# Performance work log

Hardware: AMD Instinct MI355X
Metric: run time of the kernel (lower is better)

The kernel has to match this reference:

```python
import jax, jax.numpy as jnp
import numpy as np

H, F = 4, 32          # num_of_heads, num_out_features
HF = H * F            # 128
F_IN = 128
EDGE_DIM = 64
HIDDEN = 256
B = 64
MLE = 1500
N = B * MLE           # 96000
E = 600000
LN_EPS = 1e-5


def setup_inputs() -> dict:
    key = jax.random.key(0)
    ks = jax.random.split(key, 20)

    def glorot(k, shape):
        fan_in, fan_out = shape[-2], shape[-1]
        lim = np.sqrt(6.0 / (fan_in + fan_out))
        return jax.random.uniform(k, shape, jnp.float32, -lim, lim)

    inp = {
        "in_nodes_features": jax.random.normal(ks[0], (N, F_IN), jnp.float32),
        "edge_index": jax.random.randint(ks[1], (2, E), 0, N),
        "edges": jax.random.normal(ks[2], (E, EDGE_DIM), jnp.float32),
        "instructions": jax.random.normal(ks[3], (B, HIDDEN), jnp.float32),
        "batch_ids": jax.random.randint(ks[4], (E,), 0, B),
        "max_local_entity": MLE,
        # parameters (stored as [in, out]; torch Linear is x @ W.T)
        "W_proj": glorot(ks[5], (F_IN, HF)),
        "W_edge": glorot(ks[6], (EDGE_DIM, HF)),
        "W_src_ins": glorot(ks[7], (HIDDEN, HF)),
        "b_src_ins": jnp.zeros((HF,), jnp.float32),
        "W_trg_ins": glorot(ks[8], (HIDDEN, HF)),
        "b_trg_ins": jnp.zeros((HF,), jnp.float32),
        "W_edge_ins": glorot(ks[9], (HIDDEN, HF)),
        "b_edge_ins": jnp.zeros((HF,), jnp.float32),
        "a_src": glorot(ks[10], (1, H, F)),
        "a_trg": glorot(ks[11], (1, H, F)),
        "a_edge": glorot(ks[12], (1, H, F)),
        "bias": jnp.zeros((HF,), jnp.float32),
        "W_skip": glorot(ks[13], (F_IN, HF)),
        "ln_gamma": jnp.ones((2 * HF,), jnp.float32),
        "ln_beta": jnp.zeros((2 * HF,), jnp.float32),
    }
    return inp


def _segment_softmax(scores, seg_idx, num_nodes):
    # scores: [E, H]; softmax over edges sharing the same seg_idx node
    s = scores - jax.lax.stop_gradient(scores.max())  # global-max shift, as in original
    e = jnp.exp(s)
    denom = jax.ops.segment_sum(e, seg_idx, num_segments=num_nodes)  # [N, H]
    return (e / (denom[seg_idx] + 1e-16))[..., None]  # [E, H, 1]


def _branch(proj, lift_idx, agg_idx, scores_per_edge, x, W_skip, bias, num_nodes):
    att = _segment_softmax(scores_per_edge, agg_idx, num_nodes)          # [E,H,1]
    weighted = proj[lift_idx] * att                                      # [E,H,F]
    out = jax.ops.segment_sum(weighted, agg_idx, num_segments=num_nodes) # [N,H,F]
    out = out + (x @ W_skip).reshape(num_nodes, H, F)                    # skip (F != F_in path)
    out = out.reshape(num_nodes, HF) + bias                              # concat heads + bias
    return out


def reference(in_nodes_features, edge_index, edges, instructions, batch_ids,
              max_local_entity, W_proj, W_edge, W_src_ins, b_src_ins,
              W_trg_ins, b_trg_ins, W_edge_ins, b_edge_ins,
              a_src, a_trg, a_edge, bias, W_skip, ln_gamma, ln_beta):
    x = in_nodes_features                      # dropout disabled (eval / p=0)
    num_nodes = x.shape[0]
    b = instructions.shape[0]
    src_idx, trg_idx = edge_index[0], edge_index[1]

    proj = (x @ W_proj).reshape(num_nodes, H, F)           # [N,H,F]
    eproj = (edges @ W_edge).reshape(-1, H, F)             # [E,H,F]

    def bridge(Wi, bi):  # instruction -> per-node [N,H,F]
        br = instructions @ Wi + bi                        # [B,HF]
        br = jnp.broadcast_to(br[:, None, :], (b, max_local_entity, HF))
        return br.reshape(num_nodes, H, F)

    src_br = bridge(W_src_ins, b_src_ins)
    trg_br = bridge(W_trg_ins, b_trg_ins)
    edge_br = (instructions @ W_edge_ins + b_edge_ins)[batch_ids].reshape(-1, H, F)

    scores_source = (proj * a_src * src_br).sum(-1)        # [N,H]
    scores_target = (proj * a_trg * trg_br).sum(-1)        # [N,H]
    scores_edge = (eproj * a_edge * edge_br).sum(-1)       # [E,H]

    scores_per_edge = jax.nn.leaky_relu(
        scores_source[src_idx] + scores_target[trg_idx] + scores_edge,
        negative_slope=0.2)                                # [E,H]

    # direction == 'all': aggregate src->trg and trg->src
    trg_feats = _branch(proj, src_idx, trg_idx, scores_per_edge, x, W_skip, bias, num_nodes)
    src_feats = _branch(proj, trg_idx, src_idx, scores_per_edge, x, W_skip, bias, num_nodes)

    out = jnp.concatenate([src_feats, trg_feats], axis=1)  # [N, 2*HF]
    mu = out.mean(-1, keepdims=True)
    var = ((out - mu) ** 2).mean(-1, keepdims=True)
    return (out - mu) * jax.lax.rsqrt(var + LN_EPS) * ln_gamma + ln_beta
```

## Files before the change

kernel.cpp:

```cpp
#include <hip/hip_runtime.h>
#include <stdint.h>

typedef unsigned short ushortT;
typedef __attribute__((ext_vector_type(8))) short short8;
typedef __attribute__((ext_vector_type(4))) float float4_;

#define HH 4
#define FF 32
#define HFD 128
#define F_IN 128
#define EDGE_DIM 64
#define HIDDEN 256
#define BB 64
#define MLE 1500
#define NN 96000
#define EEc 600000
#define CAP 32

__device__ __forceinline__ float bf_lo(uint32_t u){ return __uint_as_float(u << 16); }
__device__ __forceinline__ float bf_hi(uint32_t u){ return __uint_as_float(u & 0xffff0000u); }
__device__ __forceinline__ uint32_t f2bf(float f){
    uint32_t u = __float_as_uint(f);
    return (u + 0x7fffu + ((u >> 16) & 1u)) >> 16;
}
__device__ __forceinline__ short8 cvt8(const float* p){
    float4_ x0 = *(const float4_*)p;
    float4_ x1 = *(const float4_*)(p + 4);
    short8 r;
    r[0]=(short)f2bf(x0[0]); r[1]=(short)f2bf(x0[1]); r[2]=(short)f2bf(x0[2]); r[3]=(short)f2bf(x0[3]);
    r[4]=(short)f2bf(x1[0]); r[5]=(short)f2bf(x1[1]); r[6]=(short)f2bf(x1[2]); r[7]=(short)f2bf(x1[3]);
    return r;
}

__global__ void k_bridge(const float* ins, const float* Wsrc, const float* bsrc,
                         const float* Wtrg, const float* btrg,
                         const float* Wedg, const float* bedg,
                         const float* a_src, const float* a_trg, const float* a_edge,
                         const float* W_edge,
                         float* csrc, float* ctrg, float* Mout)
{
    __shared__ float ins_s[HIDDEN];
    __shared__ float ce_s[HFD];
    int b = blockIdx.x, t = threadIdx.x;
    const float* ip = ins + b * HIDDEN;
    ins_s[t]       = ip[t];
    ins_s[t + 128] = ip[t + 128];
    __syncthreads();
    float as = 0.f, at = 0.f, ae = 0.f;
    #pragma unroll 8
    for (int k = 0; k < HIDDEN; k++){
        float iv = ins_s[k];
        as += iv * Wsrc[k*HFD + t];
        at += iv * Wtrg[k*HFD + t];
        ae += iv * Wedg[k*HFD + t];
    }
    csrc[b*HFD + t] = (as + bsrc[t]) * a_src[t];
    ctrg[b*HFD + t] = (at + btrg[t]) * a_trg[t];
    ce_s[t] = (ae + bedg[t]) * a_edge[t];
    __syncthreads();
    #pragma unroll
    for (int rep = 0; rep < 2; rep++){
        int idx = t + rep * 128;
        int d = idx >> 2, h = idx & 3;
        float acc = 0.f;
        #pragma unroll
        for (int f = 0; f < FF; f++)
            acc += W_edge[d*HFD + h*FF + f] * ce_s[h*FF + f];
        Mout[b*256 + h*64 + d] = acc;
    }
}

__global__ void k_transpose(const float* Wp, const float* Wsk, ushortT* WcatT)
{
    int idx = blockIdx.x * 256 + threadIdx.x;
    int c = idx >> 7;
    int d = idx & 127;
    float v = (c < 128) ? Wp[d*128 + c] : Wsk[d*128 + (c - 128)];
    WcatT[c*128 + d] = (ushortT)f2bf(v);
}

__global__ __launch_bounds__(256) void k_gemm(const float* x, const ushortT* WcatT,
                                              const float* csrc, const float* ctrg,
                                              ushortT* proj, ushortT* skip,
                                              float* s_src, float* s_trg)
{
    int t = threadIdx.x;
    int w = t >> 6, lane = t & 63;
    int q = lane >> 4, n16 = lane & 15;
    size_t node = (size_t)blockIdx.x * 64 + w * 16 + n16;

    float4_ acc[16];
    #pragma unroll
    for (int j = 0; j < 16; j++) acc[j] = (float4_){0.f, 0.f, 0.f, 0.f};

    #pragma unroll
    for (int kk = 0; kk < 4; kk++){
        short8 bfrag = cvt8(x + node * 128 + kk*32 + q*8);
        #pragma unroll
        for (int j = 0; j < 16; j++){
            short8 afrag = *(const short8*)(WcatT + (size_t)(j*16 + n16) * 128 + kk*32 + q*8);
            acc[j] = __builtin_amdgcn_mfma_f32_16x16x32_bf16(afrag, bfrag, acc[j], 0, 0, 0);
        }
    }

    #pragma unroll
    for (int j = 0; j < 16; j++){
        uint32_t p0 = f2bf(acc[j][0]) | (f2bf(acc[j][1]) << 16);
        uint32_t p1 = f2bf(acc[j][2]) | (f2bf(acc[j][3]) << 16);
        ushortT* base = (j < 8) ? (proj + node*128 + j*16 + q*4)
                                : (skip + node*128 + (j-8)*16 + q*4);
        uint2 pv; pv.x = p0; pv.y = p1;
        *(uint2*)base = pv;
    }

    int b = (int)(node / MLE);
    const float* cs = csrc + b * HFD;
    const float* ct = ctrg + b * HFD;
    float ps[4] = {0,0,0,0}, pt[4] = {0,0,0,0};
    #pragma unroll
    for (int j = 0; j < 8; j++){
        int h = j >> 1;
        #pragma unroll
        for (int r = 0; r < 4; r++){
            int c = j*16 + q*4 + r;
            ps[h] += acc[j][r] * cs[c];
            pt[h] += acc[j][r] * ct[c];
        }
    }
    #pragma unroll
    for (int m = 16; m < 64; m <<= 1){
        #pragma unroll
        for (int hh = 0; hh < 4; hh++){
            ps[hh] += __shfl_xor(ps[hh], m, 64);
            pt[hh] += __shfl_xor(pt[hh], m, 64);
        }
    }
    float vs = (q == 0) ? ps[0] : (q == 1) ? ps[1] : (q == 2) ? ps[2] : ps[3];
    float vt = (q == 0) ? pt[0] : (q == 1) ? pt[1] : (q == 2) ? pt[2] : pt[3];
    s_src[node*4 + q] = vs;
    s_trg[node*4 + q] = vt;
}

__global__ __launch_bounds__(256) void k_score(const int* eidx, const int* bids,
    const float* edges, const float* M, const float* s_src, const float* s_trg,
    uint4* recs)
{
    int t = threadIdx.x;
    int wave = t >> 6, l = t & 63;
    int g = l >> 4, s = l & 15;
    int eb = (blockIdx.x * 4 + wave) * 16;

    int i_sel = s >> 2;
    int h_sel = s & 3;
    int e   = eb + i_sel*4 + g;
    int src = eidx[e];
    int trg = eidx[EEc + e];
    float ssv = s_src[(size_t)src*4 + h_sel];
    float stv = s_trg[(size_t)trg*4 + h_sel];

    float4_ ev[4];
    int bidv[4];
    #pragma unroll
    for (int i = 0; i < 4; i++){
        int r = i*4 + g;
        ev[i]   = *(const float4_*)(edges + (size_t)(eb + r) * 64 + s*4);
        bidv[i] = bids[eb + r];
    }

    float p00=0.f,p01=0.f,p02=0.f,p03=0.f;
    float p10=0.f,p11=0.f,p12=0.f,p13=0.f;
    float p20=0.f,p21=0.f,p22=0.f,p23=0.f;
    float p30=0.f,p31=0.f,p32=0.f,p33=0.f;
    #pragma unroll
    for (int i = 0; i < 4; i++){
        const float* Mb = M + (size_t)bidv[i] * 256;
        float4_ m0 = *(const float4_*)(Mb +   0 + s*4);
        float4_ m1 = *(const float4_*)(Mb +  64 + s*4);
        float4_ m2 = *(const float4_*)(Mb + 128 + s*4);
        float4_ m3 = *(const float4_*)(Mb + 192 + s*4);
        float4_ e4 = ev[i];
        float d0 = e4[0]*m0[0] + e4[1]*m0[1] + e4[2]*m0[2] + e4[3]*m0[3];
        float d1 = e4[0]*m1[0] + e4[1]*m1[1] + e4[2]*m1[2] + e4[3]*m1[3];
        float d2 = e4[0]*m2[0] + e4[1]*m2[1] + e4[2]*m2[2] + e4[3]*m2[3];
        float d3 = e4[0]*m3[0] + e4[1]*m3[1] + e4[2]*m3[2] + e4[3]*m3[3];
        if (i == 0){ p00=d0; p01=d1; p02=d2; p03=d3; }
        if (i == 1){ p10=d0; p11=d1; p12=d2; p13=d3; }
        if (i == 2){ p20=d0; p21=d1; p22=d2; p23=d3; }
        if (i == 3){ p30=d0; p31=d1; p32=d2; p33=d3; }
    }

    #pragma unroll
    for (int mm = 1; mm < 16; mm <<= 1){
        p00 += __shfl_xor(p00, mm, 64); p01 += __shfl_xor(p01, mm, 64);
        p02 += __shfl_xor(p02, mm, 64); p03 += __shfl_xor(p03, mm, 64);
        p10 += __shfl_xor(p10, mm, 64); p11 += __shfl_xor(p11, mm, 64);
        p12 += __shfl_xor(p12, mm, 64); p13 += __shfl_xor(p13, mm, 64);
        p20 += __shfl_xor(p20, mm, 64); p21 += __shfl_xor(p21, mm, 64);
        p22 += __shfl_xor(p22, mm, 64); p23 += __shfl_xor(p23, mm, 64);
        p30 += __shfl_xor(p30, mm, 64); p31 += __shfl_xor(p31, mm, 64);
        p32 += __shfl_xor(p32, mm, 64); p33 += __shfl_xor(p33, mm, 64);
    }

    float q0 = h_sel==0 ? p00 : h_sel==1 ? p01 : h_sel==2 ? p02 : p03;
    float q1 = h_sel==0 ? p10 : h_sel==1 ? p11 : h_sel==2 ? p12 : p13;
    float q2 = h_sel==0 ? p20 : h_sel==1 ? p21 : h_sel==2 ? p22 : p23;
    float q3 = h_sel==0 ? p30 : h_sel==1 ? p31 : h_sel==2 ? p32 : p33;
    float se = i_sel==0 ? q0 : i_sel==1 ? q1 : i_sel==2 ? q2 : q3;

    float sc = ssv + stv + se;
    sc = sc > 0.f ? sc : 0.2f * sc;
    float exv = __expf(sc);

    uint32_t my   = f2bf(exv) << ((h_sel & 1) * 16);
    uint32_t pair = my | __shfl_xor(my, 1, 64);
    uint32_t both = __shfl_xor(pair, 2, 64);

    if (h_sel == 0){
        uint4 rec;
        rec.x = (uint32_t)src; rec.y = (uint32_t)trg;
        rec.z = pair; rec.w = both;
        recs[e] = rec;
    }
}

__global__ __launch_bounds__(256) void k_build(const int* eidx,
    int* cnt_src, int* cnt_trg, uint32_t* adj_src, uint32_t* adj_trg)
{
    int e = blockIdx.x * 256 + threadIdx.x;
    if (e >= EEc) return;
    int src = eidx[e];
    int trg = eidx[EEc + e];
    int sl = atomicAdd(&cnt_src[src], 1);
    if (sl < CAP) adj_src[(size_t)src*CAP + sl] = (uint32_t)e;
    int sl2 = atomicAdd(&cnt_trg[trg], 1);
    if (sl2 < CAP) adj_trg[(size_t)trg*CAP + sl2] = (uint32_t)e;
}

__global__ __launch_bounds__(256) void k_agg(const ushortT* proj, const ushortT* skip,
    const float* bias,
    const int* cnt_src, const int* cnt_trg,
    const uint32_t* adj_src, const uint32_t* adj_trg, const uint4* recs,
    const float* gamma, const float* beta, float* out)
{
    __shared__ int   sh_nbr[2][4][CAP];
    __shared__ float sh_ev [2][4][CAP*4];

    int wave = threadIdx.x >> 6, lane = threadIdx.x & 63;
    int n = blockIdx.x * 4 + wave;
    int h = lane >> 4;

    int cnt0 = cnt_src[n]; if (cnt0 > CAP) cnt0 = CAP;
    int cnt1 = cnt_trg[n]; if (cnt1 > CAP) cnt1 = CAP;

    uint32_t e0 = 0, e1 = 0;
    if (lane < cnt0) e0 = adj_src[(size_t)n * CAP + lane];
    if (lane < cnt1) e1 = adj_trg[(size_t)n * CAP + lane];
    if (lane < cnt0){
        uint4 rec = recs[e0];
        sh_nbr[0][wave][lane] = (int)rec.y;
        float4_ evv = { bf_lo(rec.z), bf_hi(rec.z), bf_lo(rec.w), bf_hi(rec.w) };
        *(float4_*)&sh_ev[0][wave][lane*4] = evv;
    }
    if (lane < cnt1){
        uint4 rec = recs[e1];
        sh_nbr[1][wave][lane] = (int)rec.x;
        float4_ evv = { bf_lo(rec.z), bf_hi(rec.z), bf_lo(rec.w), bf_hi(rec.w) };
        *(float4_*)&sh_ev[1][wave][lane*4] = evv;
    }

    uint32_t sv = ((const uint32_t*)(skip + (size_t)n * 128))[lane];
    float b0 = bias[2*lane], b1 = bias[2*lane + 1];

    __syncthreads();

    float sk0 = bf_lo(sv) + b0;
    float sk1 = bf_hi(sv) + b1;

    float a0 = 0.f, a1 = 0.f, ad = 0.f;
    #pragma unroll 4
    for (int i = 0; i < cnt0; i++){
        int nbr  = sh_nbr[0][wave][i];
        float evw = sh_ev[0][wave][i*4 + h];
        uint32_t pv = ((const uint32_t*)(proj + (size_t)nbr * 128))[lane];
        a0 += evw * bf_lo(pv);
        a1 += evw * bf_hi(pv);
        ad += evw;
    }
    float inv = 1.f / (ad + 1e-16f);
    float f0 = a0 * inv + sk0;
    float f1 = a1 * inv + sk1;

    a0 = 0.f; a1 = 0.f; ad = 0.f;
    #pragma unroll 4
    for (int i = 0; i < cnt1; i++){
        int nbr  = sh_nbr[1][wave][i];
        float evw = sh_ev[1][wave][i*4 + h];
        uint32_t pv = ((const uint32_t*)(proj + (size_t)nbr * 128))[lane];
        a0 += evw * bf_lo(pv);
        a1 += evw * bf_hi(pv);
        ad += evw;
    }
    inv = 1.f / (ad + 1e-16f);
    float f2 = a0 * inv + sk0;
    float f3 = a1 * inv + sk1;

    float sum = f0 + f1 + f2 + f3;
    float sq  = f0*f0 + f1*f1 + f2*f2 + f3*f3;
    #pragma unroll
    for (int m = 1; m < 64; m <<= 1){
        sum += __shfl_xor(sum, m, 64);
        sq  += __shfl_xor(sq,  m, 64);
    }
    float mu  = sum * (1.f/256.f);
    float var = sq * (1.f/256.f) - mu*mu;
    var = var < 0.f ? 0.f : var;
    float rr = rsqrtf(var + 1e-5f);

    float o0 = (f0 - mu) * rr * gamma[2*lane]           + beta[2*lane];
    float o1 = (f1 - mu) * rr * gamma[2*lane + 1]       + beta[2*lane + 1];
    float o2 = (f2 - mu) * rr * gamma[128 + 2*lane]     + beta[128 + 2*lane];
    float o3 = (f3 - mu) * rr * gamma[128 + 2*lane + 1] + beta[128 + 2*lane + 1];

    float* orow = out + (size_t)n * 256;
    *(float2*)(orow + 2*lane)       = make_float2(o0, o1);
    *(float2*)(orow + 128 + 2*lane) = make_float2(o2, o3);
}

extern "C" void kernel_launch(void* const* d_in, const int* in_sizes, int n_in,
                              void* d_out, int out_size, void* d_ws, size_t ws_size,
                              hipStream_t stream)
{
    const float* x      = (const float*)d_in[0];
    const int*   eidx   = (const int*)d_in[1];
    const float* edges  = (const float*)d_in[2];
    const float* ins    = (const float*)d_in[3];
    const int*   bids   = (const int*)d_in[4];
    const float* Wproj  = (const float*)d_in[6];
    const float* Wedge  = (const float*)d_in[7];
    const float* Wsrc   = (const float*)d_in[8];
    const float* bsrc   = (const float*)d_in[9];
    const float* Wtrg   = (const float*)d_in[10];
    const float* btrg   = (const float*)d_in[11];
    const float* Wedgi  = (const float*)d_in[12];
    const float* bedgi  = (const float*)d_in[13];
    const float* a_src  = (const float*)d_in[14];
    const float* a_trg  = (const float*)d_in[15];
    const float* a_edge = (const float*)d_in[16];
    const float* bias   = (const float*)d_in[17];
    const float* Wskip  = (const float*)d_in[18];
    const float* gamma  = (const float*)d_in[19];
    const float* beta   = (const float*)d_in[20];

    char* ws = (char*)d_ws;
    size_t off = 0;
    ushortT* proj  = (ushortT*)(ws + off); off += (size_t)NN * 128 * 2;
    ushortT* skip  = (ushortT*)(ws + off); off += (size_t)NN * 128 * 2;
    ushortT* WcatT = (ushortT*)(ws + off); off += 256 * 128 * 2;
    float*   csrc  = (float*)(ws + off);   off += BB * HFD * 4;
    float*   ctrg  = (float*)(ws + off);   off += BB * HFD * 4;
    float*   M     = (float*)(ws + off);   off += BB * 256 * 4;
    float*   s_src = (float*)(ws + off);   off += (size_t)NN * 4 * 4;
    float*   s_trg = (float*)(ws + off);   off += (size_t)NN * 4 * 4;
    int*     cnt_src = (int*)(ws + off);   off += (size_t)NN * 4;
    int*     cnt_trg = (int*)(ws + off);   off += (size_t)NN * 4;
    uint32_t* adj_src = (uint32_t*)(ws + off); off += (size_t)NN * CAP * 4;
    uint32_t* adj_trg = (uint32_t*)(ws + off); off += (size_t)NN * CAP * 4;
    uint4*   recs  = (uint4*)(ws + off);   off += (size_t)EEc * 16;

    hipMemsetAsync(cnt_src, 0, (size_t)NN * 4 * 2, stream);

    k_bridge<<<dim3(BB), dim3(128), 0, stream>>>(ins, Wsrc, bsrc, Wtrg, btrg, Wedgi, bedgi,
                                                 a_src, a_trg, a_edge, Wedge, csrc, ctrg, M);
    k_transpose<<<dim3(128), dim3(256), 0, stream>>>(Wproj, Wskip, WcatT);
    k_build<<<dim3((EEc + 255)/256), dim3(256), 0, stream>>>(eidx, cnt_src, cnt_trg,
                                                             adj_src, adj_trg);
    k_gemm<<<dim3(NN/64), dim3(256), 0, stream>>>(x, WcatT, csrc, ctrg, proj, skip, s_src, s_trg);
    k_score<<<dim3(EEc/64), dim3(256), 0, stream>>>(eidx, bids, edges, M, s_src, s_trg, recs);
    k_agg<<<dim3(NN/4), dim3(256), 0, stream>>>(proj, skip, bias, cnt_src, cnt_trg,
                                                adj_src, adj_trg, recs, gamma, beta, (float*)d_out);
}
```

Measured before the change: 588.4 us.

## Replace atomic-count adjacency build with linked lists and pre-gathered transposed neighbor arrays

Removes the separate k_build pass. Instead, k_score pushes each edge onto per-node linked lists with atomicExch. A new k_walk kernel has one thread per node and direction; it traverses the list and writes neighbor ids and bf16 exp scores into column-major (slot-major) arrays. k_agg then reads those arrays directly instead of an edge index followed by a 16-byte record gather. The serial pointer chasing in k_walk has latency-bound dependent loads and uneven per-thread work. Edge order within a node also becomes nondeterministic, as before.

New measurement: 540.4 us. 8.2% less time.

```diff
diff --git a/kernel.cpp b/kernel.cpp
--- a/kernel.cpp
+++ b/kernel.cpp
@@ -143,7 +143,7 @@
 
 __global__ __launch_bounds__(256) void k_score(const int* eidx, const int* bids,
     const float* edges, const float* M, const float* s_src, const float* s_trg,
-    uint4* recs)
+    uint4* recs, int* head_src, int* head_trg, int* next_src, int* next_trg)
 {
     int t = threadIdx.x;
     int wave = t >> 6, l = t & 63;
@@ -220,26 +220,40 @@
         rec.x = (uint32_t)src; rec.y = (uint32_t)trg;
         rec.z = pair; rec.w = both;
         recs[e] = rec;
-    }
-}
-
-__global__ __launch_bounds__(256) void k_build(const int* eidx,
-    int* cnt_src, int* cnt_trg, uint32_t* adj_src, uint32_t* adj_trg)
-{
-    int e = blockIdx.x * 256 + threadIdx.x;
-    if (e >= EEc) return;
-    int src = eidx[e];
-    int trg = eidx[EEc + e];
-    int sl = atomicAdd(&cnt_src[src], 1);
-    if (sl < CAP) adj_src[(size_t)src*CAP + sl] = (uint32_t)e;
-    int sl2 = atomicAdd(&cnt_trg[trg], 1);
-    if (sl2 < CAP) adj_trg[(size_t)trg*CAP + sl2] = (uint32_t)e;
+        int old0 = atomicExch(&head_src[src], e);
+        next_src[e] = old0;
+        int old1 = atomicExch(&head_trg[trg], e);
+        next_trg[e] = old1;
+    }
+}
+
+__global__ __launch_bounds__(256) void k_walk(const int* head_src, const int* head_trg,
+    const int* next_src, const int* next_trg, const uint4* recs,
+    int* cnt_src, int* cnt_trg, uint32_t* nbrT, uint2* evT)
+{
+    int id = blockIdx.x * 256 + threadIdx.x;
+    int dir = (id >= NN) ? 1 : 0;
+    int n = id - dir * NN;
+    int e = dir ? head_trg[n] : head_src[n];
+    const int* nx = dir ? next_trg : next_src;
+    uint32_t* nT = nbrT + (size_t)dir * CAP * NN;
+    uint2*    eT = evT  + (size_t)dir * CAP * NN;
+    int c = 0;
+    while (e >= 0 && c < CAP){
+        uint4 r = recs[e];
+        int en = nx[e];
+        nT[(size_t)c*NN + n] = dir ? r.x : r.y;
+        eT[(size_t)c*NN + n] = make_uint2(r.z, r.w);
+        e = en;
+        c++;
+    }
+    if (dir) cnt_trg[n] = c; else cnt_src[n] = c;
 }
 
 __global__ __launch_bounds__(256) void k_agg(const ushortT* proj, const ushortT* skip,
     const float* bias,
     const int* cnt_src, const int* cnt_trg,
-    const uint32_t* adj_src, const uint32_t* adj_trg, const uint4* recs,
+    const uint32_t* nbrT, const uint2* evT,
     const float* gamma, const float* beta, float* out)
 {
     __shared__ int   sh_nbr[2][4][CAP];
@@ -252,19 +266,18 @@
     int cnt0 = cnt_src[n]; if (cnt0 > CAP) cnt0 = CAP;
     int cnt1 = cnt_trg[n]; if (cnt1 > CAP) cnt1 = CAP;
 
-    uint32_t e0 = 0, e1 = 0;
-    if (lane < cnt0) e0 = adj_src[(size_t)n * CAP + lane];
-    if (lane < cnt1) e1 = adj_trg[(size_t)n * CAP + lane];
     if (lane < cnt0){
-        uint4 rec = recs[e0];
-        sh_nbr[0][wave][lane] = (int)rec.y;
-        float4_ evv = { bf_lo(rec.z), bf_hi(rec.z), bf_lo(rec.w), bf_hi(rec.w) };
+        uint32_t nbr = nbrT[(size_t)lane*NN + n];
+        uint2 e2     = evT [(size_t)lane*NN + n];
+        sh_nbr[0][wave][lane] = (int)nbr;
+        float4_ evv = { bf_lo(e2.x), bf_hi(e2.x), bf_lo(e2.y), bf_hi(e2.y) };
         *(float4_*)&sh_ev[0][wave][lane*4] = evv;
     }
     if (lane < cnt1){
-        uint4 rec = recs[e1];
-        sh_nbr[1][wave][lane] = (int)rec.x;
-        float4_ evv = { bf_lo(rec.z), bf_hi(rec.z), bf_lo(rec.w), bf_hi(rec.w) };
+        uint32_t nbr = nbrT[(size_t)(CAP + lane)*NN + n];
+        uint2 e2     = evT [(size_t)(CAP + lane)*NN + n];
+        sh_nbr[1][wave][lane] = (int)nbr;
+        float4_ evv = { bf_lo(e2.x), bf_hi(e2.x), bf_lo(e2.y), bf_hi(e2.y) };
         *(float4_*)&sh_ev[1][wave][lane*4] = evv;
     }
 
@@ -363,19 +376,24 @@
     float*   s_trg = (float*)(ws + off);   off += (size_t)NN * 4 * 4;
     int*     cnt_src = (int*)(ws + off);   off += (size_t)NN * 4;
     int*     cnt_trg = (int*)(ws + off);   off += (size_t)NN * 4;
-    uint32_t* adj_src = (uint32_t*)(ws + off); off += (size_t)NN * CAP * 4;
-    uint32_t* adj_trg = (uint32_t*)(ws + off); off += (size_t)NN * CAP * 4;
+    int*     head_src = (int*)(ws + off);  off += (size_t)NN * 4;
+    int*     head_trg = (int*)(ws + off);  off += (size_t)NN * 4;
+    int*     next_src = (int*)(ws + off);  off += (size_t)EEc * 4;
+    int*     next_trg = (int*)(ws + off);  off += (size_t)EEc * 4;
     uint4*   recs  = (uint4*)(ws + off);   off += (size_t)EEc * 16;
-
-    hipMemsetAsync(cnt_src, 0, (size_t)NN * 4 * 2, stream);
+    uint32_t* nbrT = (uint32_t*)(ws + off); off += (size_t)2 * CAP * NN * 4;
+    uint2*   evT   = (uint2*)(ws + off);   off += (size_t)2 * CAP * NN * 8;
+
+    hipMemsetAsync(head_src, 0xFF, (size_t)NN * 4 * 2, stream);
 
     k_bridge<<<dim3(BB), dim3(128), 0, stream>>>(ins, Wsrc, bsrc, Wtrg, btrg, Wedgi, bedgi,
                                                  a_src, a_trg, a_edge, Wedge, csrc, ctrg, M);
     k_transpose<<<dim3(128), dim3(256), 0, stream>>>(Wproj, Wskip, WcatT);
-    k_build<<<dim3((EEc + 255)/256), dim3(256), 0, stream>>>(eidx, cnt_src, cnt_trg,
-                                                             adj_src, adj_trg);
     k_gemm<<<dim3(NN/64), dim3(256), 0, stream>>>(x, WcatT, csrc, ctrg, proj, skip, s_src, s_trg);
-    k_score<<<dim3(EEc/64), dim3(256), 0, stream>>>(eidx, bids, edges, M, s_src, s_trg, recs);
+    k_score<<<dim3(EEc/64), dim3(256), 0, stream>>>(eidx, bids, edges, M, s_src, s_trg,
+                                                    recs, head_src, head_trg, next_src, next_trg);
+    k_walk<<<dim3(2*NN/256), dim3(256), 0, stream>>>(head_src, head_trg, next_src, next_trg,
+                                                     recs, cnt_src, cnt_trg, nbrT, evT);
     k_agg<<<dim3(NN/4), dim3(256), 0, stream>>>(proj, skip, bias, cnt_src, cnt_trg,
-                                                adj_src, adj_trg, recs, gamma, beta, (float*)d_out);
-}
+                                                nbrT, evT, gamma, beta, (float*)d_out);
+}
```
